# Optimization experiments

Measured on AMD Instinct MI355X. Metric: run time of the kernel, lower is better.

Reference implementation:

```python
import math
import jax, jax.numpy as jnp
import numpy as np

PHI = (1.0 + math.sqrt(5.0)) / 2.0
LUT_N = 4096
TWO_PI = 2.0 * math.pi


def _lut_tables():
    angles = jnp.arange(LUT_N, dtype=jnp.float32) * (TWO_PI / LUT_N)
    return jnp.sin(angles), jnp.cos(angles)


def _lut_sin_cos(theta, sin_t, cos_t):
    # quantize angle to nearest LUT entry, wrap mod 2*pi
    idx = jnp.mod(jnp.round(theta * (LUT_N / TWO_PI)).astype(jnp.int32), LUT_N)
    return jnp.take(sin_t, idx), jnp.take(cos_t, idx)


def setup_inputs() -> dict:
    key = jax.random.key(0)
    ks = jax.random.split(key, 8)
    B, D, H = 4096, 4096, 16
    Dh = D // H
    return {
        'x_real': jax.random.normal(ks[0], (B, D), dtype=jnp.float32),
        'x_imag': jax.random.normal(ks[1], (B, D), dtype=jnp.float32),
        't': jax.random.uniform(ks[2], (B,), dtype=jnp.float32) * 100.0,
        'trigger_real': jax.random.normal(ks[3], (H, Dh), dtype=jnp.float32) * 0.5,
        'trigger_imag': jax.random.normal(ks[4], (H, Dh), dtype=jnp.float32) * 0.5,
        'w_query': jax.random.normal(ks[5], (H, Dh), dtype=jnp.float32) * 0.02,
        'b_query': jnp.zeros((H, Dh), dtype=jnp.float32),
        'w_out': jax.random.normal(ks[6], (D,), dtype=jnp.float32) * 0.02,
        'b_out': jnp.zeros((D,), dtype=jnp.float32),
        'beta': jnp.abs(jax.random.normal(ks[7], (D,), dtype=jnp.float32)) * 5.0 + 5.0,
    }


def reference(x_real, x_imag, t, trigger_real, trigger_imag, w_query, b_query, w_out, b_out, beta):
    sin_t, cos_t = _lut_tables()
    B, D = x_real.shape
    H, Dh = trigger_real.shape

    # ---- per-head interference (vectorized over heads) ----
    xr = x_real.reshape(B, H, Dh)
    xi = x_imag.reshape(B, H, Dh)
    t_phi_h = (t * PHI)[:, None, None]                       # (B,1,1)
    wavelength_q = 1.0 + jnp.abs(w_query)                    # (H,Dh)
    theta_r = xr / wavelength_q + b_query + t_phi_h
    theta_i = xi / wavelength_q + b_query + t_phi_h
    sin_r, cos_r = _lut_sin_cos(theta_r, sin_t, cos_t)
    sin_i, cos_i = _lut_sin_cos(theta_i, sin_t, cos_t)
    q_real = cos_r * cos_i - sin_r * sin_i                   # (B,H,Dh)
    q_imag = cos_r * sin_i + sin_r * cos_i
    int_r = (q_real * trigger_real + q_imag * trigger_imag).sum(-1)   # (B,H)
    int_i = (q_real * trigger_imag - q_imag * trigger_real).sum(-1)
    total_int_real = int_r.mean(-1)                          # (B,)
    total_int_imag = int_i.mean(-1)

    # ---- constant-Q memory update (fresh memory = zeros) ----
    beta_eff = 1.0 / (1.0 + jnp.abs(beta))                   # (D,)
    w_eff = 1.0 / (1.0 + jnp.abs(w_out))                     # (D,)
    decay = jnp.minimum(jnp.exp(-beta_eff * w_eff), 0.9999)
    int_mag = jnp.sqrt(total_int_real ** 2 + total_int_imag ** 2 + 1e-8)[:, None]  # (B,1)
    write_scale = (w_eff * (1.0 - decay))[None, :]           # (1,D)
    # initial memory is zero -> memory*decay term vanishes
    mem_real = x_real * int_mag * write_scale
    mem_imag = x_imag * int_mag * write_scale

    # ---- Euler projection of memory ----
    wavelength = 1.0 + jnp.abs(w_out)
    t_phi = (t * PHI)[:, None]
    th_or = mem_real / wavelength + b_out + t_phi
    th_oi = mem_imag / wavelength + b_out + t_phi
    sin_or, cos_or = _lut_sin_cos(th_or, sin_t, cos_t)
    sin_oi, cos_oi = _lut_sin_cos(th_oi, sin_t, cos_t)
    out_real = cos_or * cos_oi - sin_or * sin_oi
    out_imag = cos_or * sin_oi + sin_or * cos_oi
    return out_real, out_imag
```

## Files before the change

### kernel.cpp

```cpp
#include <hip/hip_runtime.h>

#define LUT_N 4096
#define DVAL  4096
#define TPB   256

static constexpr double TWO_PI_D = 6.283185307179586476925286766559;
#define PHI_F 1.61803398874989484820f

typedef float f32x4_t __attribute__((ext_vector_type(4)));

__device__ __forceinline__ float fc(const float4& f, int j) {
    switch (j) { case 0: return f.x; case 1: return f.y; case 2: return f.z; }
    return f.w;
}
__device__ __forceinline__ void sc4(float4& f, int j, float v) {
    switch (j) { case 0: f.x = v; return; case 1: f.y = v; return; case 2: f.z = v; return; }
    f.w = v;
}
__device__ __forceinline__ int lut_index(float theta, float cidx) {
    return ((int)rintf(theta * cidx)) & (LUT_N - 1);
}
__device__ __forceinline__ void nt_store4(float4 v, float4* p) {
    f32x4_t w; w.x = v.x; w.y = v.y; w.z = v.z; w.w = v.w;
    __builtin_nontemporal_store(w, (f32x4_t*)p);
}

__global__ __launch_bounds__(TPB) void echo_precompute(
    const float* __restrict__ w_query,
    const float* __restrict__ w_out,
    const float* __restrict__ beta,
    float2* __restrict__ lut,
    float*  __restrict__ wlq,
    float*  __restrict__ wlo,
    float*  __restrict__ wsc)
{
    int i = blockIdx.x * TPB + threadIdx.x;
    const float c2 = (float)(TWO_PI_D / (double)LUT_N);
    if (i < LUT_N) {
        float ang = (float)i * c2;
        lut[i] = make_float2(sinf(ang), cosf(ang));
    }
    if (i < DVAL) {
        float wavelength_q = 1.0f + fabsf(w_query[i]);
        float wavelength   = 1.0f + fabsf(w_out[i]);
        float beta_eff = 1.0f / (1.0f + fabsf(beta[i]));
        float w_eff    = 1.0f / wavelength;
        float decay    = fminf(expf(-beta_eff * w_eff), 0.9999f);
        wlq[i] = wavelength_q;
        wlo[i] = wavelength;
        wsc[i] = w_eff * (1.0f - decay);
    }
}

template<bool USE_WS>
__global__ __launch_bounds__(TPB) void echo_main(
    const float* __restrict__ x_real,
    const float* __restrict__ x_imag,
    const float* __restrict__ t,
    const float* __restrict__ trig_r,
    const float* __restrict__ trig_i,
    const float* __restrict__ w_query,
    const float* __restrict__ b_query,
    const float* __restrict__ w_out,
    const float* __restrict__ b_out,
    const float* __restrict__ beta,
    const float2* __restrict__ lutG,
    const float*  __restrict__ wlqG,
    const float*  __restrict__ wloG,
    const float*  __restrict__ wscG,
    float* __restrict__ out,
    int B)
{
    __shared__ float2 lutS[LUT_N];
    __shared__ float redR[4], redI[4];
    __shared__ float magS;

    const int tid = threadIdx.x;
    const int b   = blockIdx.x;
    const float cidx = (float)((double)LUT_N / TWO_PI_D);

    if constexpr (USE_WS) {
        const float4* src = (const float4*)lutG;
        float4* dst = (float4*)lutS;
        #pragma unroll
        for (int k = 0; k < 8; ++k) {
            int idx = tid + TPB * k;
            dst[idx] = src[idx];
        }
    } else {
        const float c2 = (float)(TWO_PI_D / (double)LUT_N);
        #pragma unroll
        for (int k = 0; k < 16; ++k) {
            int idx = tid + TPB * k;
            float ang = (float)idx * c2;
            lutS[idx] = make_float2(sinf(ang), cosf(ang));
        }
    }

    const float tphi = t[b] * PHI_F;
    const float* xr = x_real + (size_t)b * DVAL;
    const float* xi = x_imag + (size_t)b * DVAL;

    float4 xr_s[4], xi_s[4];
    float accr = 0.0f, acci = 0.0f;

    __syncthreads();

    #pragma unroll
    for (int k = 0; k < 4; ++k) {
        int v = tid + TPB * k;
        float4 a = ((const float4*)xr)[v];
        float4 c = ((const float4*)xi)[v];
        xr_s[k] = a; xi_s[k] = c;

        float4 wl4;
        if constexpr (USE_WS) {
            wl4 = ((const float4*)wlqG)[v];
        } else {
            float4 wq4 = ((const float4*)w_query)[v];
            wl4 = make_float4(1.0f + fabsf(wq4.x), 1.0f + fabsf(wq4.y),
                              1.0f + fabsf(wq4.z), 1.0f + fabsf(wq4.w));
        }
        float4 bq4 = ((const float4*)b_query)[v];
        float4 tr4 = ((const float4*)trig_r)[v];
        float4 ti4 = ((const float4*)trig_i)[v];

        #pragma unroll
        for (int j = 0; j < 4; ++j) {
            float wl = fc(wl4, j), bq = fc(bq4, j);
            float thr = fc(a, j) / wl + bq + tphi;
            float thi = fc(c, j) / wl + bq + tphi;
            int ir = lut_index(thr, cidx);
            int ii = lut_index(thi, cidx);
            float2 s = lutS[(ir + ii) & (LUT_N - 1)];
            float q_r = s.y, q_i = s.x;
            accr += q_r * fc(tr4, j) + q_i * fc(ti4, j);
            acci += q_r * fc(ti4, j) - q_i * fc(tr4, j);
        }
    }

    #pragma unroll
    for (int m = 32; m >= 1; m >>= 1) {
        accr += __shfl_xor(accr, m, 64);
        acci += __shfl_xor(acci, m, 64);
    }
    if ((tid & 63) == 0) { redR[tid >> 6] = accr; redI[tid >> 6] = acci; }
    __syncthreads();
    if (tid == 0) {
        float tr = (redR[0] + redR[1] + redR[2] + redR[3]) * 0.0625f;
        float ti = (redI[0] + redI[1] + redI[2] + redI[3]) * 0.0625f;
        magS = sqrtf(tr * tr + ti * ti + 1e-8f);
    }
    __syncthreads();
    const float mag = magS;

    float4* outR = (float4*)(out + (size_t)b * DVAL);
    float4* outI = (float4*)(out + (size_t)B * DVAL + (size_t)b * DVAL);

    #pragma unroll
    for (int k = 0; k < 4; ++k) {
        int v = tid + TPB * k;
        float4 wl4, ws4;
        if constexpr (USE_WS) {
            wl4 = ((const float4*)wloG)[v];
            ws4 = ((const float4*)wscG)[v];
        } else {
            float4 wo4 = ((const float4*)w_out)[v];
            float4 be4 = ((const float4*)beta)[v];
            #pragma unroll
            for (int j = 0; j < 4; ++j) {
                float wavelength = 1.0f + fabsf(fc(wo4, j));
                float beta_eff = 1.0f / (1.0f + fabsf(fc(be4, j)));
                float w_eff = 1.0f / wavelength;
                float decay = fminf(expf(-beta_eff * w_eff), 0.9999f);
                sc4(wl4, j, wavelength);
                sc4(ws4, j, w_eff * (1.0f - decay));
            }
        }
        float4 bo4 = ((const float4*)b_out)[v];

        float4 oR, oI;
        #pragma unroll
        for (int j = 0; j < 4; ++j) {
            float ws = fc(ws4, j), wl = fc(wl4, j), bo = fc(bo4, j);
            float mr = (fc(xr_s[k], j) * mag) * ws;
            float mi = (fc(xi_s[k], j) * mag) * ws;
            float thr = mr / wl + bo + tphi;
            float thi = mi / wl + bo + tphi;
            int ir = lut_index(thr, cidx);
            int ii = lut_index(thi, cidx);
            float2 s = lutS[(ir + ii) & (LUT_N - 1)];
            sc4(oR, j, s.y);
            sc4(oI, j, s.x);
        }
        nt_store4(oR, &outR[v]);
        nt_store4(oI, &outI[v]);
    }
}

extern "C" void kernel_launch(void* const* d_in, const int* in_sizes, int n_in,
                              void* d_out, int out_size, void* d_ws, size_t ws_size,
                              hipStream_t stream) {
    const float* x_real    = (const float*)d_in[0];
    const float* x_imag    = (const float*)d_in[1];
    const float* t         = (const float*)d_in[2];
    const float* trig_r    = (const float*)d_in[3];
    const float* trig_i    = (const float*)d_in[4];
    const float* w_query   = (const float*)d_in[5];
    const float* b_query   = (const float*)d_in[6];
    const float* w_out     = (const float*)d_in[7];
    const float* b_out     = (const float*)d_in[8];
    const float* beta      = (const float*)d_in[9];
    float* out = (float*)d_out;

    const int B = in_sizes[2];
    const size_t need = (size_t)LUT_N * sizeof(float2) + 3 * (size_t)DVAL * sizeof(float);

    if (d_ws != nullptr && ws_size >= need) {
        char* ws = (char*)d_ws;
        float2* lut = (float2*)ws;
        float*  wlq = (float*)(ws + (size_t)LUT_N * sizeof(float2));
        float*  wlo = wlq + DVAL;
        float*  wsc = wlo + DVAL;
        echo_precompute<<<(LUT_N > DVAL ? LUT_N : DVAL) / TPB, TPB, 0, stream>>>(
            w_query, w_out, beta, lut, wlq, wlo, wsc);
        echo_main<true><<<B, TPB, 0, stream>>>(
            x_real, x_imag, t, trig_r, trig_i, w_query, b_query, w_out, b_out, beta,
            lut, wlq, wlo, wsc, out, B);
    } else {
        echo_main<false><<<B, TPB, 0, stream>>>(
            x_real, x_imag, t, trig_r, trig_i, w_query, b_query, w_out, b_out, beta,
            nullptr, nullptr, nullptr, nullptr, out, B);
    }
}
```

Measured before the change: 266.6 us.

## Process two batch rows per block to amortize shared LUT loading

Doubles the block size to 512 threads, with each half handling a separate batch row, so the 32KB sine/cosine LUT copied into shared memory serves two rows. This halves the grid and the per-row LUT fill traffic and synchronization overhead. Per-half reductions are kept separate, and odd B is handled by clamping the row index (duplicate writes). Larger blocks may reduce scheduling flexibility and raise register pressure under the new launch bound.

```diff
diff --git a/kernel.cpp b/kernel.cpp
--- a/kernel.cpp
+++ b/kernel.cpp
@@ -2,7 +2,7 @@
 
 #define LUT_N 4096
 #define DVAL  4096
-#define TPB   256
+#define TPB   512
 
 static constexpr double TWO_PI_D = 6.283185307179586476925286766559;
 #define PHI_F 1.61803398874989484820f
@@ -25,7 +25,7 @@
     __builtin_nontemporal_store(w, (f32x4_t*)p);
 }
 
-__global__ __launch_bounds__(TPB) void echo_precompute(
+__global__ __launch_bounds__(256) void echo_precompute(
     const float* __restrict__ w_query,
     const float* __restrict__ w_out,
     const float* __restrict__ beta,
@@ -34,7 +34,7 @@
     float*  __restrict__ wlo,
     float*  __restrict__ wsc)
 {
-    int i = blockIdx.x * TPB + threadIdx.x;
+    int i = blockIdx.x * 256 + threadIdx.x;
     const float c2 = (float)(TWO_PI_D / (double)LUT_N);
     if (i < LUT_N) {
         float ang = (float)i * c2;
@@ -53,7 +53,7 @@
 }
 
 template<bool USE_WS>
-__global__ __launch_bounds__(TPB) void echo_main(
+__global__ __launch_bounds__(TPB, 8) void echo_main(
     const float* __restrict__ x_real,
     const float* __restrict__ x_imag,
     const float* __restrict__ t,
@@ -72,34 +72,37 @@
     int B)
 {
     __shared__ float2 lutS[LUT_N];
-    __shared__ float redR[4], redI[4];
-    __shared__ float magS;
-
-    const int tid = threadIdx.x;
-    const int b   = blockIdx.x;
+    __shared__ float redR[8], redI[8];
+    __shared__ float magS[2];
+
+    const int tid  = threadIdx.x;
+    const int half = tid >> 8;
+    const int lane = tid & 255;
+    int row = blockIdx.x * 2 + half;
+    if (row >= B) row = B - 1;
     const float cidx = (float)((double)LUT_N / TWO_PI_D);
 
     if constexpr (USE_WS) {
         const float4* src = (const float4*)lutG;
         float4* dst = (float4*)lutS;
         #pragma unroll
-        for (int k = 0; k < 8; ++k) {
+        for (int k = 0; k < 4; ++k) {
             int idx = tid + TPB * k;
             dst[idx] = src[idx];
         }
     } else {
         const float c2 = (float)(TWO_PI_D / (double)LUT_N);
         #pragma unroll
-        for (int k = 0; k < 16; ++k) {
+        for (int k = 0; k < 8; ++k) {
             int idx = tid + TPB * k;
             float ang = (float)idx * c2;
             lutS[idx] = make_float2(sinf(ang), cosf(ang));
         }
     }
 
-    const float tphi = t[b] * PHI_F;
-    const float* xr = x_real + (size_t)b * DVAL;
-    const float* xi = x_imag + (size_t)b * DVAL;
+    const float tphi = t[row] * PHI_F;
+    const float* xr = x_real + (size_t)row * DVAL;
+    const float* xi = x_imag + (size_t)row * DVAL;
 
     float4 xr_s[4], xi_s[4];
     float accr = 0.0f, acci = 0.0f;
@@ -108,7 +111,7 @@
 
     #pragma unroll
     for (int k = 0; k < 4; ++k) {
-        int v = tid + TPB * k;
+        int v = lane + 256 * k;
         float4 a = ((const float4*)xr)[v];
         float4 c = ((const float4*)xi)[v];
         xr_s[k] = a; xi_s[k] = c;
@@ -144,22 +147,24 @@
         accr += __shfl_xor(accr, m, 64);
         acci += __shfl_xor(acci, m, 64);
     }
-    if ((tid & 63) == 0) { redR[tid >> 6] = accr; redI[tid >> 6] = acci; }
+    const int wave = tid >> 6;
+    if ((tid & 63) == 0) { redR[wave] = accr; redI[wave] = acci; }
     __syncthreads();
-    if (tid == 0) {
-        float tr = (redR[0] + redR[1] + redR[2] + redR[3]) * 0.0625f;
-        float ti = (redI[0] + redI[1] + redI[2] + redI[3]) * 0.0625f;
-        magS = sqrtf(tr * tr + ti * ti + 1e-8f);
+    if (lane == 0) {
+        int o = half * 4;
+        float tr = (redR[o] + redR[o+1] + redR[o+2] + redR[o+3]) * 0.0625f;
+        float ti = (redI[o] + redI[o+1] + redI[o+2] + redI[o+3]) * 0.0625f;
+        magS[half] = sqrtf(tr * tr + ti * ti + 1e-8f);
     }
     __syncthreads();
-    const float mag = magS;
-
-    float4* outR = (float4*)(out + (size_t)b * DVAL);
-    float4* outI = (float4*)(out + (size_t)B * DVAL + (size_t)b * DVAL);
+    const float mag = magS[half];
+
+    float4* outR = (float4*)(out + (size_t)row * DVAL);
+    float4* outI = (float4*)(out + (size_t)B * DVAL + (size_t)row * DVAL);
 
     #pragma unroll
     for (int k = 0; k < 4; ++k) {
-        int v = tid + TPB * k;
+        int v = lane + 256 * k;
         float4 wl4, ws4;
         if constexpr (USE_WS) {
             wl4 = ((const float4*)wloG)[v];
@@ -214,6 +219,7 @@
     float* out = (float*)d_out;
 
     const int B = in_sizes[2];
+    const int nblocks = (B + 1) / 2;
     const size_t need = (size_t)LUT_N * sizeof(float2) + 3 * (size_t)DVAL * sizeof(float);
 
     if (d_ws != nullptr && ws_size >= need) {
@@ -222,13 +228,13 @@
         float*  wlq = (float*)(ws + (size_t)LUT_N * sizeof(float2));
         float*  wlo = wlq + DVAL;
         float*  wsc = wlo + DVAL;
-        echo_precompute<<<(LUT_N > DVAL ? LUT_N : DVAL) / TPB, TPB, 0, stream>>>(
+        echo_precompute<<<(LUT_N > DVAL ? LUT_N : DVAL) / 256, 256, 0, stream>>>(
             w_query, w_out, beta, lut, wlq, wlo, wsc);
-        echo_main<true><<<B, TPB, 0, stream>>>(
+        echo_main<true><<<nblocks, TPB, 0, stream>>>(
             x_real, x_imag, t, trig_r, trig_i, w_query, b_query, w_out, b_out, beta,
             lut, wlq, wlo, wsc, out, B);
     } else {
-        echo_main<false><<<B, TPB, 0, stream>>>(
+        echo_main<false><<<nblocks, TPB, 0, stream>>>(
             x_real, x_imag, t, trig_r, trig_i, w_query, b_query, w_out, b_out, beta,
             nullptr, nullptr, nullptr, nullptr, out, B);
     }
```

After: 265.7 us. No clear change (-0.3%).
